# Optimization experiments

Hardware: AMD Instinct MI355X
Metric: run time of the kernel (lower is better)

## Reference

```python
import jax, jax.numpy as jnp
import numpy as np

B, T, TR, DIM, H = 1, 4096, 1024, 1536, 12
DH = DIM // H          # 128
EPS = 1e-6             # RMSNorm eps
REF_SCALE = 1.0


def setup_inputs() -> dict:
    key = jax.random.key(0)
    ks = jax.random.split(key, 20)
    s = 0.02
    w = lambda k: jax.random.normal(k, (DIM, DIM), jnp.float32) * s
    b = lambda k: jax.random.normal(k, (DIM,), jnp.float32) * 0.01
    theta = jax.random.uniform(ks[2], (T, DH // 2), jnp.float32) * (2.0 * np.pi)
    return {
        "hidden_states": jax.random.normal(ks[0], (B, T, DIM), jnp.float32),
        "ref_hidden_states": jax.random.normal(ks[1], (B, TR, DIM), jnp.float32),
        "rot_cos": jnp.cos(theta),
        "rot_sin": jnp.sin(theta),
        "Wq": w(ks[3]), "bq": b(ks[4]),
        "Wk": w(ks[5]), "bk": b(ks[6]),
        "Wv": w(ks[7]), "bv": b(ks[8]),
        "Wkr": w(ks[9]), "bkr": b(ks[10]),
        "Wvr": w(ks[11]), "bvr": b(ks[12]),
        "Wo": w(ks[13]), "bo": b(ks[14]),
        "gq": jnp.ones((DIM,), jnp.float32),
        "gk": jnp.ones((DIM,), jnp.float32),
    }


def _rmsnorm(x, g):
    return x * jax.lax.rsqrt(jnp.mean(x * x, axis=-1, keepdims=True) + EPS) * g


def _heads(x):  # [B, T, DIM] -> [B, H, T, DH]
    return x.reshape(B, -1, H, DH).transpose(0, 2, 1, 3)


def _merge(x):  # [B, H, T, DH] -> [B, T, DIM]
    return x.transpose(0, 2, 1, 3).reshape(B, -1, DIM)


def _rope(x, c, s):
    # consecutive pairs along DH form complex numbers (view_as_complex semantics)
    xe, xo = x[..., 0::2], x[..., 1::2]
    c = c[None, None]  # [1,1,T,DH/2]
    s = s[None, None]
    re = xe * c - xo * s
    im = xe * s + xo * c
    return jnp.stack([re, im], axis=-1).reshape(x.shape)


def _attn(q, k, v):
    scale = 1.0 / jnp.sqrt(jnp.asarray(DH, q.dtype))
    p = jax.nn.softmax(jnp.einsum("bhqd,bhkd->bhqk", q, k) * scale, axis=-1)
    return jnp.einsum("bhqk,bhkd->bhqd", p, v)


def reference(hidden_states, ref_hidden_states, rot_cos, rot_sin,
              Wq, bq, Wk, bk, Wv, bv, Wkr, bkr, Wvr, bvr, Wo, bo, gq, gk):
    # QKV projections (self-attention: encoder_hidden_states = hidden_states)
    q_lin = hidden_states @ Wq + bq
    k_lin = hidden_states @ Wk + bk
    v_lin = hidden_states @ Wv + bv

    # ---- reference-attention branch (uses pre-RoPE query) ----
    ref_q = _heads(_rmsnorm(q_lin, gq))
    ref_k = _heads(_rmsnorm(ref_hidden_states @ Wkr + bkr, gk))
    ref_v = _heads(ref_hidden_states @ Wvr + bvr)
    ref_out = _merge(_attn(ref_q, ref_k, ref_v))  # [B, T, DIM]

    # ---- main attention with QK-norm + RoPE ----
    q = _rope(_heads(_rmsnorm(q_lin, gq)), rot_cos, rot_sin)
    k = _rope(_heads(_rmsnorm(k_lin, gk)), rot_cos, rot_sin)
    v = _heads(v_lin)
    main_out = _merge(_attn(q, k, v))  # [B, T, DIM]

    # scaled residual combine + output projection (dropout = identity)
    out = main_out + REF_SCALE * ref_out
    return out @ Wo + bo
```

## Files before the change

kernel.cpp:

```cpp
#include <hip/hip_runtime.h>

typedef unsigned short u16;
typedef unsigned int u32;
typedef __attribute__((ext_vector_type(8))) short short8;
typedef __attribute__((ext_vector_type(4))) float f32x4;

__device__ inline u16 f2b(float f) {
  u32 u = __builtin_bit_cast(u32, f);
  u += 0x7fff + ((u >> 16) & 1);
  return (u16)(u >> 16);
}
__device__ inline float b2f(u16 u) {
  return __builtin_bit_cast(float, (u32)u << 16);
}
__device__ inline void c_store(float* p, float v) { *p = v; }
__device__ inline void c_store(u16* p, float v) { *p = f2b(v); }

__device__ inline float fexp2(float x) {
#if __has_builtin(__builtin_amdgcn_exp2f)
  return __builtin_amdgcn_exp2f(x);
#else
  return exp2f(x);
#endif
}

typedef const __attribute__((address_space(1))) u32 gu32;
typedef __attribute__((address_space(3))) u32 lu32;
__device__ inline void async16(const u16* g, u16* l) {
  __builtin_amdgcn_global_load_lds((gu32*)g, (lu32*)l, 16, 0, 0);
}

#define QS (0.08838834764831843f * 1.4426950408889634f)

template <typename TC>
__global__ __launch_bounds__(256) void gemm128_kernel(
    const u16* __restrict__ A, long lda,
    const u16* __restrict__ Bt, long ldb,
    TC* __restrict__ C0, TC* __restrict__ C1, TC* __restrict__ C2, long ldc,
    const float* b0, const float* b1, const float* b2,
    int K) {
  __shared__ u16 As[128 * 32];
  __shared__ u16 Bs[128 * 32];

  const int tid = threadIdx.x;
  const int lane = tid & 63;
  const int w = tid >> 6;
  const int r = lane & 15;
  const int quad = lane >> 4;
  const int m0 = blockIdx.y * 128;
  const int nb = blockIdx.x * 128;
  const int seg = nb / 1536;
  const int nc = nb - seg * 1536;
  TC* C = seg == 0 ? C0 : (seg == 1 ? C1 : C2);
  const float* bias = seg == 0 ? b0 : (seg == 1 ? b1 : b2);

  const int srow = lane >> 2;
  const int sx = ((lane & 3) ^ (srow & 3)) * 8;
  const u16* Ag = A + (size_t)(m0 + w * 32 + srow) * lda + sx;
  const u16* Bg = Bt + (size_t)(nb + w * 32 + srow) * ldb + sx;
  u16* const Al0 = &As[(w * 32) * 32];
  u16* const Al1 = &As[(w * 32 + 16) * 32];
  u16* const Bl0 = &Bs[(w * 32) * 32];
  u16* const Bl1 = &Bs[(w * 32 + 16) * 32];

  const int wm = (w >> 1) * 64;
  const int wn = (w & 1) * 64;

  f32x4 acc[4][4];
#pragma unroll
  for (int i = 0; i < 4; ++i)
#pragma unroll
    for (int j = 0; j < 4; ++j) acc[i][j] = (f32x4){0.f, 0.f, 0.f, 0.f};

  const int fco = (quad ^ (r & 3)) * 8;

  for (int kk = 0; kk < K; kk += 32) {
    __syncthreads();
    async16(Ag + kk, Al0);
    async16(Ag + kk + 16 * lda, Al1);
    async16(Bg + kk, Bl0);
    async16(Bg + kk + 16 * ldb, Bl1);
    __syncthreads();

    short8 af[4], bf[4];
#pragma unroll
    for (int mi = 0; mi < 4; ++mi)
      af[mi] = *reinterpret_cast<const short8*>(&As[(wm + 16 * mi + r) * 32 + fco]);
#pragma unroll
    for (int ni = 0; ni < 4; ++ni)
      bf[ni] = *reinterpret_cast<const short8*>(&Bs[(wn + 16 * ni + r) * 32 + fco]);
#pragma unroll
    for (int mi = 0; mi < 4; ++mi)
#pragma unroll
      for (int ni = 0; ni < 4; ++ni)
        acc[mi][ni] = __builtin_amdgcn_mfma_f32_16x16x32_bf16(af[mi], bf[ni], acc[mi][ni], 0, 0, 0);
  }

#pragma unroll
  for (int mi = 0; mi < 4; ++mi)
#pragma unroll
    for (int ni = 0; ni < 4; ++ni)
#pragma unroll
      for (int rr = 0; rr < 4; ++rr) {
        const int row = m0 + wm + 16 * mi + 4 * quad + rr;
        const int col = nc + wn + 16 * ni + r;
        c_store(&C[(size_t)row * ldc + col], acc[mi][ni][rr] + bias[col]);
      }
}

__global__ __launch_bounds__(256) void conv2_kernel(
    const float* __restrict__ xa, u16* __restrict__ ya, int n8a,
    const float* __restrict__ xb, u16* __restrict__ yb, int n8b) {
  int i = blockIdx.x * 256 + threadIdx.x;
  const float* x;
  u16* y;
  if (i < n8a) {
    x = xa; y = ya;
  } else {
    i -= n8a;
    if (i >= n8b) return;
    x = xb; y = yb;
  }
  const float4 v0 = reinterpret_cast<const float4*>(x)[2 * i];
  const float4 v1 = reinterpret_cast<const float4*>(x)[2 * i + 1];
  uint4 rv;
  rv.x = (u32)f2b(v0.x) | ((u32)f2b(v0.y) << 16);
  rv.y = (u32)f2b(v0.z) | ((u32)f2b(v0.w) << 16);
  rv.z = (u32)f2b(v1.x) | ((u32)f2b(v1.y) << 16);
  rv.w = (u32)f2b(v1.z) | ((u32)f2b(v1.w) << 16);
  reinterpret_cast<uint4*>(y)[i] = rv;
}

__device__ inline void transconv_body(const float* __restrict__ W, u16* __restrict__ Wt) {
  __shared__ u16 Ls[64 * 72];
  const int tid = threadIdx.x;
  const int k0 = blockIdx.y * 64;
  const int n0 = blockIdx.x * 64;
#pragma unroll
  for (int i = 0; i < 4; ++i) {
    const int c = tid + 256 * i;
    const int row = c >> 4;
    const int c4 = (c & 15) * 4;
    const float4 v = *reinterpret_cast<const float4*>(&W[(size_t)(k0 + row) * 1536 + n0 + c4]);
    Ls[(c4 + 0) * 72 + row] = f2b(v.x);
    Ls[(c4 + 1) * 72 + row] = f2b(v.y);
    Ls[(c4 + 2) * 72 + row] = f2b(v.z);
    Ls[(c4 + 3) * 72 + row] = f2b(v.w);
  }
  __syncthreads();
#pragma unroll
  for (int i = 0; i < 2; ++i) {
    const int c = tid + 256 * i;
    const int n = c >> 3;
    const int kc = (c & 7) * 8;
    u16 tmp[8];
#pragma unroll
    for (int j = 0; j < 8; ++j) tmp[j] = Ls[n * 72 + kc + j];
    *reinterpret_cast<uint4*>(&Wt[(size_t)(n0 + n) * 1536 + k0 + kc]) =
        *reinterpret_cast<const uint4*>(tmp);
  }
}

__global__ __launch_bounds__(256) void transconv5_kernel(
    const float* W0, const float* W1, const float* W2, const float* W3, const float* W4,
    u16* T0, u16* T1, u16* T2, u16* T3, u16* T4) {
  const int z = blockIdx.z;
  const float* W = z == 0 ? W0 : z == 1 ? W1 : z == 2 ? W2 : z == 3 ? W3 : W4;
  u16* Wt = z == 0 ? T0 : z == 1 ? T1 : z == 2 ? T2 : z == 3 ? T3 : T4;
  transconv_body(W, Wt);
}

__global__ __launch_bounds__(256) void transconv_kernel(
    const float* __restrict__ W, u16* __restrict__ Wt) {
  transconv_body(W, Wt);
}

__global__ __launch_bounds__(256) void rmsnorm3_kernel(
    const u16* xq, const u16* xk, const u16* xkr,
    const float* gq, const float* gk,
    const float* rc, const float* rs,
    u16* oq_plain, u16* oq_rope, u16* ok_rope, u16* okr_plain) {
  __shared__ float red[4];
  const int z = blockIdx.y;
  const int row = blockIdx.x;
  if (z == 2 && row >= 1024) return;
  const u16* x; const float* g; u16* po; u16* pr; float sc;
  if (z == 0)      { x = xq;  g = gq; po = oq_plain; pr = oq_rope; sc = QS;  }
  else if (z == 1) { x = xk;  g = gk; po = nullptr;  pr = ok_rope; sc = 1.f; }
  else             { x = xkr; g = gk; po = okr_plain; pr = nullptr; sc = 1.f; }

  const int tid = threadIdx.x;
  const u32* xr = reinterpret_cast<const u32*>(x + (size_t)row * 1536);
  float xe[3], xo[3];
  float ss = 0.f;
#pragma unroll
  for (int j = 0; j < 3; ++j) {
    const u32 u = xr[tid + 256 * j];
    const float e = b2f((u16)(u & 0xffff));
    const float o = b2f((u16)(u >> 16));
    xe[j] = e; xo[j] = o;
    ss += e * e + o * o;
  }
#pragma unroll
  for (int off = 32; off; off >>= 1) ss += __shfl_xor(ss, off, 64);
  if ((tid & 63) == 0) red[tid >> 6] = ss;
  __syncthreads();
  const float total = red[0] + red[1] + red[2] + red[3];
  const float rinv = rsqrtf(total * (1.0f / 1536.0f) + 1e-6f) * sc;
  u32* po32 = po ? reinterpret_cast<u32*>(po + (size_t)row * 1536) : nullptr;
  u32* pr32 = pr ? reinterpret_cast<u32*>(pr + (size_t)row * 1536) : nullptr;
#pragma unroll
  for (int j = 0; j < 3; ++j) {
    const int p = tid + 256 * j;
    const float2 gg = reinterpret_cast<const float2*>(g)[p];
    const float e = xe[j] * rinv * gg.x;
    const float o = xo[j] * rinv * gg.y;
    if (po32) po32[p] = (u32)f2b(e) | ((u32)f2b(o) << 16);
    if (pr32) {
      const int i = p & 63;
      const float c = rc[row * 64 + i];
      const float s = rs[row * 64 + i];
      const float re = e * c - o * s;
      const float im = e * s + o * c;
      pr32[p] = (u32)f2b(re) | ((u32)f2b(im) << 16);
    }
  }
}

__global__ __launch_bounds__(256) void vtrans2_kernel(
    const u16* __restrict__ V0, u16* __restrict__ Vt0,
    const u16* __restrict__ V1, u16* __restrict__ Vt1) {
  __shared__ u16 Ls[64 * 136];
  const int z = blockIdx.z;
  const int kvLen = z == 0 ? 4096 : 1024;
  const int kv0 = blockIdx.x * 64;
  if (kv0 >= kvLen) return;
  const u16* V = z == 0 ? V0 : V1;
  u16* Vt = z == 0 ? Vt0 : Vt1;
  const int tid = threadIdx.x;
  const int h = blockIdx.y;
#pragma unroll
  for (int i = 0; i < 4; ++i) {
    const int c = tid + 256 * i;
    const int row = c >> 4, c8 = c & 15;
    *reinterpret_cast<uint4*>(&Ls[row * 136 + 8 * c8]) =
        *reinterpret_cast<const uint4*>(V + (size_t)(kv0 + row) * 1536 + h * 128 + 8 * c8);
  }
  __syncthreads();
#pragma unroll
  for (int i = 0; i < 4; ++i) {
    const int c = tid + 256 * i;
    const int d = c >> 3, kc = c & 7;
    u16 tmp[8];
#pragma unroll
    for (int j = 0; j < 8; ++j) tmp[j] = Ls[(8 * kc + j) * 136 + d];
    *reinterpret_cast<uint4*>(Vt + ((size_t)h * 128 + d) * kvLen + kv0 + 8 * kc) =
        *reinterpret_cast<const uint4*>(tmp);
  }
}

__global__ __launch_bounds__(256) void flash_kernel(
    const u16* __restrict__ Q, const u16* __restrict__ K,
    const u16* __restrict__ Vt, float* __restrict__ O,
    u16* __restrict__ Ob, int kvLen, int addO) {
  __shared__ u16 Ks[64 * 128];
  __shared__ u16 Vs[128 * 64];
  __shared__ u16 Pb[4][16 * 72];
  __shared__ float ab[4][16];

  const int tid = threadIdx.x;
  const int lane = tid & 63;
  const int w = tid >> 6;
  const int r = lane & 15;
  const int quad = lane >> 4;
  const int h = blockIdx.y;
  const int q0 = blockIdx.x * 64;
  const int qrow = q0 + 16 * w + r;

  short8 qf[4];
  const u16* qbase = Q + (size_t)qrow * 1536 + h * 128 + 8 * quad;
#pragma unroll
  for (int ks = 0; ks < 4; ++ks)
    qf[ks] = *reinterpret_cast<const short8*>(qbase + 32 * ks);

  const u16* Vth = Vt + (size_t)h * 128 * kvLen;
  const u16* kg[4]; u16* kl[4];
  const u16* vg[4]; u16* vl[4];
  {
    const int p16 = lane & 15, rin = lane >> 4;
    const int p8 = lane & 7, din = lane >> 3;
#pragma unroll
    for (int j = 0; j < 4; ++j) {
      const int row = 16 * w + 4 * j + rin;
      kg[j] = K + (size_t)row * 1536 + h * 128 + 8 * (p16 ^ (row & 15));
      kl[j] = &Ks[(16 * w + 4 * j) * 128];
      const int d = 32 * w + 8 * j + din;
      vg[j] = Vth + (size_t)d * kvLen + 8 * (p8 ^ (d & 7));
      vl[j] = &Vs[(32 * w + 8 * j) * 64];
    }
  }

  f32x4 Oc[8];
#pragma unroll
  for (int dt = 0; dt < 8; ++dt) Oc[dt] = (f32x4){0.f, 0.f, 0.f, 0.f};
  float m_i = -1e30f, l_i = 0.f;

  for (int k0 = 0; k0 < kvLen; k0 += 64) {
    __syncthreads();
#pragma unroll
    for (int j = 0; j < 4; ++j) async16(kg[j] + (size_t)k0 * 1536, kl[j]);
#pragma unroll
    for (int j = 0; j < 4; ++j) async16(vg[j] + k0, vl[j]);
    __syncthreads();

    f32x4 St[4];
#pragma unroll
    for (int mt = 0; mt < 4; ++mt) St[mt] = (f32x4){0.f, 0.f, 0.f, 0.f};
#pragma unroll
    for (int mt = 0; mt < 4; ++mt) {
      const u16* kp = &Ks[(16 * mt + r) * 128];
#pragma unroll
      for (int ks = 0; ks < 4; ++ks) {
        const short8 af = *reinterpret_cast<const short8*>(kp + 8 * ((quad + 4 * ks) ^ r));
        St[mt] = __builtin_amdgcn_mfma_f32_16x16x32_bf16(af, qf[ks], St[mt], 0, 0, 0);
      }
    }

    float mloc = -1e30f;
#pragma unroll
    for (int mt = 0; mt < 4; ++mt)
#pragma unroll
      for (int rr = 0; rr < 4; ++rr) mloc = fmaxf(mloc, St[mt][rr]);
    mloc = fmaxf(mloc, __shfl_xor(mloc, 16, 64));
    mloc = fmaxf(mloc, __shfl_xor(mloc, 32, 64));
    const float mn = fmaxf(m_i, mloc);

    float alpha = 1.0f;
    if (__any(mloc > m_i)) {
      alpha = fexp2(m_i - mn);
      if (quad == 0) ab[w][r] = alpha;
      const float4 a4 = *reinterpret_cast<const float4*>(&ab[w][4 * quad]);
#pragma unroll
      for (int dt = 0; dt < 8; ++dt) {
        Oc[dt][0] *= a4.x; Oc[dt][1] *= a4.y; Oc[dt][2] *= a4.z; Oc[dt][3] *= a4.w;
      }
    }

    float psum = 0.f;
    uint2 pk[4];
#pragma unroll
    for (int mt = 0; mt < 4; ++mt) {
      const float p0 = fexp2(St[mt][0] - mn);
      const float p1 = fexp2(St[mt][1] - mn);
      const float p2 = fexp2(St[mt][2] - mn);
      const float p3 = fexp2(St[mt][3] - mn);
      psum += (p0 + p1) + (p2 + p3);
      pk[mt].x = (u32)f2b(p0) | ((u32)f2b(p1) << 16);
      pk[mt].y = (u32)f2b(p2) | ((u32)f2b(p3) << 16);
    }
    psum += __shfl_xor(psum, 16, 64);
    psum += __shfl_xor(psum, 32, 64);
    l_i = l_i * alpha + psum;
    m_i = mn;

#pragma unroll
    for (int mt = 0; mt < 4; ++mt)
      *reinterpret_cast<uint2*>(&Pb[w][r * 72 + 16 * mt + 4 * quad]) = pk[mt];

    const short8 pa0 = *reinterpret_cast<const short8*>(&Pb[w][r * 72 + 8 * quad]);
    const short8 pa1 = *reinterpret_cast<const short8*>(&Pb[w][r * 72 + 32 + 8 * quad]);

    const int sw = r & 7;
#pragma unroll
    for (int dt = 0; dt < 8; ++dt) {
      const int d = 16 * dt + r;
      const short8 b0 = *reinterpret_cast<const short8*>(&Vs[d * 64 + 8 * (quad ^ sw)]);
      const short8 b1 = *reinterpret_cast<const short8*>(&Vs[d * 64 + 8 * ((4 + quad) ^ sw)]);
      Oc[dt] = __builtin_amdgcn_mfma_f32_16x16x32_bf16(pa0, b0, Oc[dt], 0, 0, 0);
      Oc[dt] = __builtin_amdgcn_mfma_f32_16x16x32_bf16(pa1, b1, Oc[dt], 0, 0, 0);
    }
  }

  if (quad == 0) ab[w][r] = 1.0f / l_i;
  const float4 li4 = *reinterpret_cast<const float4*>(&ab[w][4 * quad]);
  const float lv[4] = {li4.x, li4.y, li4.z, li4.w};
  float* obf = O + (size_t)(q0 + 16 * w) * 1536 + h * 128;
  u16* obb = Ob + (size_t)(q0 + 16 * w) * 1536 + h * 128;
#pragma unroll
  for (int rr = 0; rr < 4; ++rr) {
    float* orow = obf + (size_t)(4 * quad + rr) * 1536 + r;
    u16* brow = obb + (size_t)(4 * quad + rr) * 1536 + r;
#pragma unroll
    for (int dt = 0; dt < 8; ++dt) {
      float v = Oc[dt][rr] * lv[rr];
      if (addO) {
        v += orow[16 * dt];
        brow[16 * dt] = f2b(v);
      } else {
        orow[16 * dt] = v;
      }
    }
  }
}

extern "C" void kernel_launch(void* const* d_in, const int* in_sizes, int n_in,
                              void* d_out, int out_size, void* d_ws, size_t ws_size,
                              hipStream_t stream) {
  (void)in_sizes; (void)n_in; (void)out_size; (void)ws_size;
  constexpr int T = 4096, TR = 1024, DIM = 1536, NH = 12;

  const float* hs  = (const float*)d_in[0];
  const float* rhs = (const float*)d_in[1];
  const float* rc  = (const float*)d_in[2];
  const float* rs  = (const float*)d_in[3];
  const float* Wq  = (const float*)d_in[4];
  const float* bq  = (const float*)d_in[5];
  const float* Wk  = (const float*)d_in[6];
  const float* bk  = (const float*)d_in[7];
  const float* Wv  = (const float*)d_in[8];
  const float* bv  = (const float*)d_in[9];
  const float* Wkr = (const float*)d_in[10];
  const float* bkr = (const float*)d_in[11];
  const float* Wvr = (const float*)d_in[12];
  const float* bvr = (const float*)d_in[13];
  const float* Wo  = (const float*)d_in[14];
  const float* bo  = (const float*)d_in[15];
  const float* gq  = (const float*)d_in[16];
  const float* gk  = (const float*)d_in[17];
  float* out = (float*)d_out;

  char* ws = (char*)d_ws;
  size_t off = 0;
  auto alloc = [&](size_t bytes) -> void* {
    void* p = ws + off;
    off += (bytes + 255) & ~(size_t)255;
    return p;
  };
  u16* bQ    = (u16*)alloc((size_t)T * DIM * 2);
  u16* bQr   = (u16*)alloc((size_t)T * DIM * 2);
  u16* bK    = (u16*)alloc((size_t)T * DIM * 2);
  u16* bV    = (u16*)alloc((size_t)T * DIM * 2);
  u16* bKr   = (u16*)alloc((size_t)TR * DIM * 2);
  u16* bVr   = (u16*)alloc((size_t)TR * DIM * 2);
  float* bO  = (float*)alloc((size_t)T * DIM * 4);
  u16* bHs   = (u16*)alloc((size_t)T * DIM * 2);
  u16* bRhs  = (u16*)alloc((size_t)TR * DIM * 2);
  u16* bWqkv = (u16*)alloc((size_t)3 * DIM * DIM * 2);
  u16* bWr   = (u16*)alloc((size_t)2 * DIM * DIM * 2);
  u16* VtG = bHs;
  u16* VtR = bRhs;
  u16* bOb = bWqkv;
  u16* bWoT = bWr;

  const dim3 blk(256);

  conv2_kernel<<<dim3((T * DIM / 8 + TR * DIM / 8 + 255) / 256), blk, 0, stream>>>(
      hs, bHs, T * DIM / 8, rhs, bRhs, TR * DIM / 8);

  transconv5_kernel<<<dim3(24, 24, 5), blk, 0, stream>>>(
      Wq, Wk, Wv, Wkr, Wvr,
      bWqkv + 0 * (size_t)DIM * DIM, bWqkv + 1 * (size_t)DIM * DIM,
      bWqkv + 2 * (size_t)DIM * DIM, bWr + 0 * (size_t)DIM * DIM,
      bWr + 1 * (size_t)DIM * DIM);

  gemm128_kernel<u16><<<dim3(36, 32), blk, 0, stream>>>(
      bHs, DIM, bWqkv, DIM, bQ, bK, bV, DIM, bq, bk, bv, DIM);
  gemm128_kernel<u16><<<dim3(24, 8), blk, 0, stream>>>(
      bRhs, DIM, bWr, DIM, bKr, bVr, (u16*)nullptr, DIM, bkr, bvr, nullptr, DIM);

  transconv_kernel<<<dim3(24, 24), blk, 0, stream>>>(Wo, bWoT);

  rmsnorm3_kernel<<<dim3(T, 3), blk, 0, stream>>>(
      bQ, bK, bKr, gq, gk, rc, rs, bQ, bQr, bK, bKr);

  vtrans2_kernel<<<dim3(T / 64, NH, 2), blk, 0, stream>>>(bV, VtG, bVr, VtR);

  flash_kernel<<<dim3(T / 64, NH), blk, 0, stream>>>(bQ, bKr, VtR, bO, bOb, TR, 0);
  flash_kernel<<<dim3(T / 64, NH), blk, 0, stream>>>(bQr, bK, VtG, bO, bOb, T, 1);

  gemm128_kernel<float><<<dim3(12, 32), blk, 0, stream>>>(
      bOb, DIM, bWoT, DIM, out, (float*)nullptr, (float*)nullptr, DIM, bo, nullptr, nullptr, DIM);
}
```

Baseline: 568.9 us.

## Fuse both attention passes into one double-buffered flash kernel, shrink small GEMM tiles

Merges the reference-attention and main-attention launches into one kernel that runs both phases per block and keeps the first phase's normalized output in registers. This removes the fp32 intermediate O buffer and its write and readback. K/V tile loads become double-buffered, so the next tile's async loads overlap the current tile's compute, at the cost of doubled LDS. The GEMM M-tile is templated, and the smaller GEMMs use 64-row tiles to launch more blocks. P is packed to bf16 with cheaper rounding that does not do ties-to-even.

```diff
diff --git a/kernel.cpp b/kernel.cpp
--- a/kernel.cpp
+++ b/kernel.cpp
@@ -12,6 +12,11 @@
 }
 __device__ inline float b2f(u16 u) {
   return __builtin_bit_cast(float, (u32)u << 16);
+}
+__device__ inline u32 pack_bf16_rn(float a, float b) {
+  const u32 ua = __builtin_bit_cast(u32, a) + 0x8000u;
+  const u32 ub = __builtin_bit_cast(u32, b) + 0x8000u;
+  return (ua >> 16) | (ub & 0xffff0000u);
 }
 __device__ inline void c_store(float* p, float v) { *p = v; }
 __device__ inline void c_store(u16* p, float v) { *p = f2b(v); }
@@ -32,14 +37,14 @@
 
 #define QS (0.08838834764831843f * 1.4426950408889634f)
 
-template <typename TC>
+template <int MI, typename TC>
 __global__ __launch_bounds__(256) void gemm128_kernel(
     const u16* __restrict__ A, long lda,
     const u16* __restrict__ Bt, long ldb,
     TC* __restrict__ C0, TC* __restrict__ C1, TC* __restrict__ C2, long ldc,
     const float* b0, const float* b1, const float* b2,
     int K) {
-  __shared__ u16 As[128 * 32];
+  __shared__ u16 As[32 * MI * 32];
   __shared__ u16 Bs[128 * 32];
 
   const int tid = threadIdx.x;
@@ -47,7 +52,7 @@
   const int w = tid >> 6;
   const int r = lane & 15;
   const int quad = lane >> 4;
-  const int m0 = blockIdx.y * 128;
+  const int m0 = blockIdx.y * (32 * MI);
   const int nb = blockIdx.x * 128;
   const int seg = nb / 1536;
   const int nc = nb - seg * 1536;
@@ -56,19 +61,20 @@
 
   const int srow = lane >> 2;
   const int sx = ((lane & 3) ^ (srow & 3)) * 8;
-  const u16* Ag = A + (size_t)(m0 + w * 32 + srow) * lda + sx;
+  const u16* Ag = A + (size_t)(m0 + w * 8 * MI + srow) * lda + sx;
   const u16* Bg = Bt + (size_t)(nb + w * 32 + srow) * ldb + sx;
-  u16* const Al0 = &As[(w * 32) * 32];
-  u16* const Al1 = &As[(w * 32 + 16) * 32];
+  u16* Al[MI / 2];
+#pragma unroll
+  for (int j = 0; j < MI / 2; ++j) Al[j] = &As[(w * 8 * MI + 16 * j) * 32];
   u16* const Bl0 = &Bs[(w * 32) * 32];
   u16* const Bl1 = &Bs[(w * 32 + 16) * 32];
 
-  const int wm = (w >> 1) * 64;
+  const int wm = (w >> 1) * (16 * MI);
   const int wn = (w & 1) * 64;
 
-  f32x4 acc[4][4];
-#pragma unroll
-  for (int i = 0; i < 4; ++i)
+  f32x4 acc[MI][4];
+#pragma unroll
+  for (int i = 0; i < MI; ++i)
 #pragma unroll
     for (int j = 0; j < 4; ++j) acc[i][j] = (f32x4){0.f, 0.f, 0.f, 0.f};
 
@@ -76,28 +82,28 @@
 
   for (int kk = 0; kk < K; kk += 32) {
     __syncthreads();
-    async16(Ag + kk, Al0);
-    async16(Ag + kk + 16 * lda, Al1);
+#pragma unroll
+    for (int j = 0; j < MI / 2; ++j) async16(Ag + kk + (size_t)(16 * j) * lda, Al[j]);
     async16(Bg + kk, Bl0);
     async16(Bg + kk + 16 * ldb, Bl1);
     __syncthreads();
 
-    short8 af[4], bf[4];
-#pragma unroll
-    for (int mi = 0; mi < 4; ++mi)
+    short8 af[MI], bf[4];
+#pragma unroll
+    for (int mi = 0; mi < MI; ++mi)
       af[mi] = *reinterpret_cast<const short8*>(&As[(wm + 16 * mi + r) * 32 + fco]);
 #pragma unroll
     for (int ni = 0; ni < 4; ++ni)
       bf[ni] = *reinterpret_cast<const short8*>(&Bs[(wn + 16 * ni + r) * 32 + fco]);
 #pragma unroll
-    for (int mi = 0; mi < 4; ++mi)
+    for (int mi = 0; mi < MI; ++mi)
 #pragma unroll
       for (int ni = 0; ni < 4; ++ni)
         acc[mi][ni] = __builtin_amdgcn_mfma_f32_16x16x32_bf16(af[mi], bf[ni], acc[mi][ni], 0, 0, 0);
   }
 
 #pragma unroll
-  for (int mi = 0; mi < 4; ++mi)
+  for (int mi = 0; mi < MI; ++mi)
 #pragma unroll
     for (int ni = 0; ni < 4; ++ni)
 #pragma unroll
@@ -259,12 +265,12 @@
   }
 }
 
-__global__ __launch_bounds__(256) void flash_kernel(
-    const u16* __restrict__ Q, const u16* __restrict__ K,
-    const u16* __restrict__ Vt, float* __restrict__ O,
-    u16* __restrict__ Ob, int kvLen, int addO) {
-  __shared__ u16 Ks[64 * 128];
-  __shared__ u16 Vs[128 * 64];
+__global__ __launch_bounds__(256) void flash2_kernel(
+    const u16* __restrict__ Qc, const u16* __restrict__ Kc, const u16* __restrict__ Vtc,
+    const u16* __restrict__ Qm, const u16* __restrict__ Km, const u16* __restrict__ Vtm,
+    u16* __restrict__ Ob) {
+  __shared__ u16 Ks[2][64 * 128];
+  __shared__ u16 Vs[2][128 * 64];
   __shared__ u16 Pb[4][16 * 72];
   __shared__ float ab[4][16];
 
@@ -276,128 +282,153 @@
   const int h = blockIdx.y;
   const int q0 = blockIdx.x * 64;
   const int qrow = q0 + 16 * w + r;
-
-  short8 qf[4];
-  const u16* qbase = Q + (size_t)qrow * 1536 + h * 128 + 8 * quad;
-#pragma unroll
-  for (int ks = 0; ks < 4; ++ks)
-    qf[ks] = *reinterpret_cast<const short8*>(qbase + 32 * ks);
-
-  const u16* Vth = Vt + (size_t)h * 128 * kvLen;
-  const u16* kg[4]; u16* kl[4];
-  const u16* vg[4]; u16* vl[4];
-  {
-    const int p16 = lane & 15, rin = lane >> 4;
-    const int p8 = lane & 7, din = lane >> 3;
-#pragma unroll
-    for (int j = 0; j < 4; ++j) {
-      const int row = 16 * w + 4 * j + rin;
-      kg[j] = K + (size_t)row * 1536 + h * 128 + 8 * (p16 ^ (row & 15));
-      kl[j] = &Ks[(16 * w + 4 * j) * 128];
-      const int d = 32 * w + 8 * j + din;
-      vg[j] = Vth + (size_t)d * kvLen + 8 * (p8 ^ (d & 7));
-      vl[j] = &Vs[(32 * w + 8 * j) * 64];
+  const int sw = r & 7;
+
+  f32x4 Ox[8];
+#pragma unroll
+  for (int dt = 0; dt < 8; ++dt) Ox[dt] = (f32x4){0.f, 0.f, 0.f, 0.f};
+
+  for (int ph = 0; ph < 2; ++ph) {
+    const u16* Q  = ph ? Qm : Qc;
+    const u16* K  = ph ? Km : Kc;
+    const u16* Vt = ph ? Vtm : Vtc;
+    const int kvLen = ph ? 4096 : 1024;
+    const int nt = kvLen >> 6;
+
+    short8 qf[4];
+    {
+      const u16* qbase = Q + (size_t)qrow * 1536 + h * 128 + 8 * quad;
+#pragma unroll
+      for (int ks = 0; ks < 4; ++ks)
+        qf[ks] = *reinterpret_cast<const short8*>(qbase + 32 * ks);
     }
-  }
-
-  f32x4 Oc[8];
-#pragma unroll
-  for (int dt = 0; dt < 8; ++dt) Oc[dt] = (f32x4){0.f, 0.f, 0.f, 0.f};
-  float m_i = -1e30f, l_i = 0.f;
-
-  for (int k0 = 0; k0 < kvLen; k0 += 64) {
+
+    const u16* Vth = Vt + (size_t)h * 128 * kvLen;
+    const u16* kg[4]; const u16* vg[4];
+    int klo[4], vlo[4];
+    {
+      const int p16 = lane & 15, rin = lane >> 4;
+      const int p8 = lane & 7, din = lane >> 3;
+#pragma unroll
+      for (int j = 0; j < 4; ++j) {
+        const int row = 16 * w + 4 * j + rin;
+        kg[j] = K + (size_t)row * 1536 + h * 128 + 8 * (p16 ^ (row & 15));
+        klo[j] = (16 * w + 4 * j) * 128;
+        const int d = 32 * w + 8 * j + din;
+        vg[j] = Vth + (size_t)d * kvLen + 8 * (p8 ^ (d & 7));
+        vlo[j] = (32 * w + 8 * j) * 64;
+      }
+    }
+
+    f32x4 Oc[8];
+#pragma unroll
+    for (int dt = 0; dt < 8; ++dt) Oc[dt] = (f32x4){0.f, 0.f, 0.f, 0.f};
+    float m_i = -1e30f, l_i = 0.f;
+
     __syncthreads();
 #pragma unroll
-    for (int j = 0; j < 4; ++j) async16(kg[j] + (size_t)k0 * 1536, kl[j]);
-#pragma unroll
-    for (int j = 0; j < 4; ++j) async16(vg[j] + k0, vl[j]);
-    __syncthreads();
-
-    f32x4 St[4];
-#pragma unroll
-    for (int mt = 0; mt < 4; ++mt) St[mt] = (f32x4){0.f, 0.f, 0.f, 0.f};
-#pragma unroll
-    for (int mt = 0; mt < 4; ++mt) {
-      const u16* kp = &Ks[(16 * mt + r) * 128];
-#pragma unroll
-      for (int ks = 0; ks < 4; ++ks) {
-        const short8 af = *reinterpret_cast<const short8*>(kp + 8 * ((quad + 4 * ks) ^ r));
-        St[mt] = __builtin_amdgcn_mfma_f32_16x16x32_bf16(af, qf[ks], St[mt], 0, 0, 0);
-      }
+    for (int j = 0; j < 4; ++j) async16(kg[j], &Ks[0][klo[j]]);
+#pragma unroll
+    for (int j = 0; j < 4; ++j) async16(vg[j], &Vs[0][vlo[j]]);
+
+    int buf = 0;
+    for (int t = 0; t < nt; ++t) {
+      __syncthreads();
+      if (t + 1 < nt) {
+        const size_t ko = (size_t)(t + 1) * 64 * 1536;
+        const int vo = (t + 1) * 64;
+#pragma unroll
+        for (int j = 0; j < 4; ++j) async16(kg[j] + ko, &Ks[buf ^ 1][klo[j]]);
+#pragma unroll
+        for (int j = 0; j < 4; ++j) async16(vg[j] + vo, &Vs[buf ^ 1][vlo[j]]);
+      }
+      const u16* Ksb = Ks[buf];
+      const u16* Vsb = Vs[buf];
+
+      f32x4 St[4];
+#pragma unroll
+      for (int mt = 0; mt < 4; ++mt) St[mt] = (f32x4){0.f, 0.f, 0.f, 0.f};
+#pragma unroll
+      for (int mt = 0; mt < 4; ++mt) {
+        const u16* kp = &Ksb[(16 * mt + r) * 128];
+#pragma unroll
+        for (int ks = 0; ks < 4; ++ks) {
+          const short8 af = *reinterpret_cast<const short8*>(kp + 8 * ((quad + 4 * ks) ^ r));
+          St[mt] = __builtin_amdgcn_mfma_f32_16x16x32_bf16(af, qf[ks], St[mt], 0, 0, 0);
+        }
+      }
+
+      float mloc = -1e30f;
+#pragma unroll
+      for (int mt = 0; mt < 4; ++mt)
+#pragma unroll
+        for (int rr = 0; rr < 4; ++rr) mloc = fmaxf(mloc, St[mt][rr]);
+      mloc = fmaxf(mloc, __shfl_xor(mloc, 16, 64));
+      mloc = fmaxf(mloc, __shfl_xor(mloc, 32, 64));
+      const float mn = fmaxf(m_i, mloc);
+
+      float alpha = 1.0f;
+      if (__any(mloc > m_i)) {
+        alpha = fexp2(m_i - mn);
+        if (quad == 0) ab[w][r] = alpha;
+        const float4 a4 = *reinterpret_cast<const float4*>(&ab[w][4 * quad]);
+#pragma unroll
+        for (int dt = 0; dt < 8; ++dt) {
+          Oc[dt][0] *= a4.x; Oc[dt][1] *= a4.y; Oc[dt][2] *= a4.z; Oc[dt][3] *= a4.w;
+        }
+      }
+
+      float psum = 0.f;
+      uint2 pk[4];
+#pragma unroll
+      for (int mt = 0; mt < 4; ++mt) {
+        const float p0 = fexp2(St[mt][0] - mn);
+        const float p1 = fexp2(St[mt][1] - mn);
+        const float p2 = fexp2(St[mt][2] - mn);
+        const float p3 = fexp2(St[mt][3] - mn);
+        psum += (p0 + p1) + (p2 + p3);
+        pk[mt].x = pack_bf16_rn(p0, p1);
+        pk[mt].y = pack_bf16_rn(p2, p3);
+      }
+      psum += __shfl_xor(psum, 16, 64);
+      psum += __shfl_xor(psum, 32, 64);
+      l_i = l_i * alpha + psum;
+      m_i = mn;
+
+#pragma unroll
+      for (int mt = 0; mt < 4; ++mt)
+        *reinterpret_cast<uint2*>(&Pb[w][r * 72 + 16 * mt + 4 * quad]) = pk[mt];
+
+      const short8 pa0 = *reinterpret_cast<const short8*>(&Pb[w][r * 72 + 8 * quad]);
+      const short8 pa1 = *reinterpret_cast<const short8*>(&Pb[w][r * 72 + 32 + 8 * quad]);
+
+#pragma unroll
+      for (int dt = 0; dt < 8; ++dt) {
+        const int d = 16 * dt + r;
+        const short8 b0 = *reinterpret_cast<const short8*>(&Vsb[d * 64 + 8 * (quad ^ sw)]);
+        const short8 b1 = *reinterpret_cast<const short8*>(&Vsb[d * 64 + 8 * ((4 + quad) ^ sw)]);
+        Oc[dt] = __builtin_amdgcn_mfma_f32_16x16x32_bf16(pa0, b0, Oc[dt], 0, 0, 0);
+        Oc[dt] = __builtin_amdgcn_mfma_f32_16x16x32_bf16(pa1, b1, Oc[dt], 0, 0, 0);
+      }
+      buf ^= 1;
     }
 
-    float mloc = -1e30f;
-#pragma unroll
-    for (int mt = 0; mt < 4; ++mt)
-#pragma unroll
-      for (int rr = 0; rr < 4; ++rr) mloc = fmaxf(mloc, St[mt][rr]);
-    mloc = fmaxf(mloc, __shfl_xor(mloc, 16, 64));
-    mloc = fmaxf(mloc, __shfl_xor(mloc, 32, 64));
-    const float mn = fmaxf(m_i, mloc);
-
-    float alpha = 1.0f;
-    if (__any(mloc > m_i)) {
-      alpha = fexp2(m_i - mn);
-      if (quad == 0) ab[w][r] = alpha;
-      const float4 a4 = *reinterpret_cast<const float4*>(&ab[w][4 * quad]);
-#pragma unroll
-      for (int dt = 0; dt < 8; ++dt) {
-        Oc[dt][0] *= a4.x; Oc[dt][1] *= a4.y; Oc[dt][2] *= a4.z; Oc[dt][3] *= a4.w;
-      }
-    }
-
-    float psum = 0.f;
-    uint2 pk[4];
-#pragma unroll
-    for (int mt = 0; mt < 4; ++mt) {
-      const float p0 = fexp2(St[mt][0] - mn);
-      const float p1 = fexp2(St[mt][1] - mn);
-      const float p2 = fexp2(St[mt][2] - mn);
-      const float p3 = fexp2(St[mt][3] - mn);
-      psum += (p0 + p1) + (p2 + p3);
-      pk[mt].x = (u32)f2b(p0) | ((u32)f2b(p1) << 16);
-      pk[mt].y = (u32)f2b(p2) | ((u32)f2b(p3) << 16);
-    }
-    psum += __shfl_xor(psum, 16, 64);
-    psum += __shfl_xor(psum, 32, 64);
-    l_i = l_i * alpha + psum;
-    m_i = mn;
-
-#pragma unroll
-    for (int mt = 0; mt < 4; ++mt)
-      *reinterpret_cast<uint2*>(&Pb[w][r * 72 + 16 * mt + 4 * quad]) = pk[mt];
-
-    const short8 pa0 = *reinterpret_cast<const short8*>(&Pb[w][r * 72 + 8 * quad]);
-    const short8 pa1 = *reinterpret_cast<const short8*>(&Pb[w][r * 72 + 32 + 8 * quad]);
-
-    const int sw = r & 7;
-#pragma unroll
-    for (int dt = 0; dt < 8; ++dt) {
-      const int d = 16 * dt + r;
-      const short8 b0 = *reinterpret_cast<const short8*>(&Vs[d * 64 + 8 * (quad ^ sw)]);
-      const short8 b1 = *reinterpret_cast<const short8*>(&Vs[d * 64 + 8 * ((4 + quad) ^ sw)]);
-      Oc[dt] = __builtin_amdgcn_mfma_f32_16x16x32_bf16(pa0, b0, Oc[dt], 0, 0, 0);
-      Oc[dt] = __builtin_amdgcn_mfma_f32_16x16x32_bf16(pa1, b1, Oc[dt], 0, 0, 0);
-    }
-  }
-
-  if (quad == 0) ab[w][r] = 1.0f / l_i;
-  const float4 li4 = *reinterpret_cast<const float4*>(&ab[w][4 * quad]);
-  const float lv[4] = {li4.x, li4.y, li4.z, li4.w};
-  float* obf = O + (size_t)(q0 + 16 * w) * 1536 + h * 128;
-  u16* obb = Ob + (size_t)(q0 + 16 * w) * 1536 + h * 128;
-#pragma unroll
-  for (int rr = 0; rr < 4; ++rr) {
-    float* orow = obf + (size_t)(4 * quad + rr) * 1536 + r;
-    u16* brow = obb + (size_t)(4 * quad + rr) * 1536 + r;
-#pragma unroll
-    for (int dt = 0; dt < 8; ++dt) {
-      float v = Oc[dt][rr] * lv[rr];
-      if (addO) {
-        v += orow[16 * dt];
-        brow[16 * dt] = f2b(v);
-      } else {
-        orow[16 * dt] = v;
+    if (quad == 0) ab[w][r] = 1.0f / l_i;
+    const float4 li4 = *reinterpret_cast<const float4*>(&ab[w][4 * quad]);
+    const float lv[4] = {li4.x, li4.y, li4.z, li4.w};
+    if (ph == 0) {
+#pragma unroll
+      for (int dt = 0; dt < 8; ++dt)
+#pragma unroll
+        for (int rr = 0; rr < 4; ++rr) Ox[dt][rr] = Oc[dt][rr] * lv[rr];
+    } else {
+      u16* obb = Ob + (size_t)(q0 + 16 * w) * 1536 + h * 128;
+#pragma unroll
+      for (int rr = 0; rr < 4; ++rr) {
+        u16* brow = obb + (size_t)(4 * quad + rr) * 1536 + r;
+#pragma unroll
+        for (int dt = 0; dt < 8; ++dt)
+          brow[16 * dt] = f2b(Oc[dt][rr] * lv[rr] + Ox[dt][rr]);
       }
     }
   }
@@ -442,7 +473,6 @@
   u16* bV    = (u16*)alloc((size_t)T * DIM * 2);
   u16* bKr   = (u16*)alloc((size_t)TR * DIM * 2);
   u16* bVr   = (u16*)alloc((size_t)TR * DIM * 2);
-  float* bO  = (float*)alloc((size_t)T * DIM * 4);
   u16* bHs   = (u16*)alloc((size_t)T * DIM * 2);
   u16* bRhs  = (u16*)alloc((size_t)TR * DIM * 2);
   u16* bWqkv = (u16*)alloc((size_t)3 * DIM * DIM * 2);
@@ -463,9 +493,9 @@
       bWqkv + 2 * (size_t)DIM * DIM, bWr + 0 * (size_t)DIM * DIM,
       bWr + 1 * (size_t)DIM * DIM);
 
-  gemm128_kernel<u16><<<dim3(36, 32), blk, 0, stream>>>(
+  gemm128_kernel<4, u16><<<dim3(36, 32), blk, 0, stream>>>(
       bHs, DIM, bWqkv, DIM, bQ, bK, bV, DIM, bq, bk, bv, DIM);
-  gemm128_kernel<u16><<<dim3(24, 8), blk, 0, stream>>>(
+  gemm128_kernel<2, u16><<<dim3(24, 16), blk, 0, stream>>>(
       bRhs, DIM, bWr, DIM, bKr, bVr, (u16*)nullptr, DIM, bkr, bvr, nullptr, DIM);
 
   transconv_kernel<<<dim3(24, 24), blk, 0, stream>>>(Wo, bWoT);
@@ -475,9 +505,9 @@
 
   vtrans2_kernel<<<dim3(T / 64, NH, 2), blk, 0, stream>>>(bV, VtG, bVr, VtR);
 
-  flash_kernel<<<dim3(T / 64, NH), blk, 0, stream>>>(bQ, bKr, VtR, bO, bOb, TR, 0);
-  flash_kernel<<<dim3(T / 64, NH), blk, 0, stream>>>(bQr, bK, VtG, bO, bOb, T, 1);
-
-  gemm128_kernel<float><<<dim3(12, 32), blk, 0, stream>>>(
+  flash2_kernel<<<dim3(T / 64, NH), blk, 0, stream>>>(
+      bQ, bKr, VtR, bQr, bK, VtG, bOb);
+
+  gemm128_kernel<2, float><<<dim3(12, 64), blk, 0, stream>>>(
       bOb, DIM, bWoT, DIM, out, (float*)nullptr, (float*)nullptr, DIM, bo, nullptr, nullptr, DIM);
 }
```

Result: slower. 721.8 us (+26.9%).
